# Kernel optimization log

Hardware: AMD Instinct MI355X
Metric: run time of the kernel (lower is better)

Reference implementation:

```python
import jax, jax.numpy as jnp
import numpy as np

DIM, WIDTH, TOTAL, BATCH, NSLOTS = 4096, 4, 16384, 8, 256


def setup_inputs() -> dict:
    key = jax.random.key(0)
    ks = jax.random.split(key, 6)
    x = jax.random.normal(ks[0], (DIM, TOTAL), dtype=jnp.float32)
    weight = jax.random.normal(ks[1], (DIM, WIDTH), dtype=jnp.float32) * 0.1
    conv_states = jax.random.normal(ks[2], (NSLOTS, DIM, WIDTH - 1), dtype=jnp.float32)
    cuts = jnp.sort(jax.random.randint(ks[3], (BATCH - 1,), 1, TOTAL)).astype(jnp.int32)
    query_start_loc = jnp.concatenate([
        jnp.zeros((1,), jnp.int32), cuts, jnp.full((1,), TOTAL, jnp.int32)])
    cache_indices = jax.random.permutation(ks[4], NSLOTS)[:BATCH].astype(jnp.int32)
    initial_state_mode = jax.random.randint(ks[5], (BATCH,), 0, 2).astype(jnp.int32)
    return dict(x=x, weight=weight, conv_states=conv_states,
                query_start_loc=query_start_loc, cache_indices=cache_indices,
                initial_state_mode=initial_state_mode,
                pad_slot_id=-1, residual_connection=1)


def _causal_conv1d_varlen(x, weight, conv_states, qsl, cache_indices, init_mode,
                          pad_slot_id, residual_connection):
    dim, T = x.shape
    width = weight.shape[1]
    state_len = width - 1
    nslots = conv_states.shape[0]
    B = qsl.shape[0] - 1

    t = jnp.arange(T)
    # sequence id and local position of every packed token
    seg = jnp.clip(jnp.searchsorted(qsl, t, side='right') - 1, 0, B - 1)  # [T]
    p = t - qsl[seg]                                                      # [T] local pos
    raw_slot = cache_indices[seg]
    valid_slot = raw_slot != pad_slot_id
    slot = jnp.where(valid_slot, raw_slot, 0)
    use_init = (init_mode[seg] != 0) & valid_slot                         # [T]

    # depthwise causal conv: out[:,t] = sum_k w[:,k] * concat(init_state, x_seq)[:, p+k]
    out = jnp.zeros_like(x)
    for k in range(width):
        d = width - 1 - k  # lookback distance
        if d == 0:
            val = x
        else:
            in_seq = p >= d
            vx = x[:, jnp.clip(t - d, 0, T - 1)]                          # [dim,T]
            st_idx = jnp.clip(state_len - d + p, 0, state_len - 1)        # [T]
            vs = conv_states[slot, :, st_idx].T                           # [dim,T]
            val = jnp.where(in_seq[None, :], vx,
                            jnp.where(use_init[None, :], vs, 0.0))
        out = out + weight[:, k:k + 1] * val

    if residual_connection:
        out = out + x

    # updated cache: last state_len entries of concat(init_state, x_seq) per sequence
    j = jnp.arange(state_len)                                             # [S]
    start, end = qsl[:-1], qsl[1:]
    L = end - start                                                       # [B]
    gx = end[:, None] + j[None, :] - state_len                            # [B,S] global idx
    from_x = gx >= start[:, None]                                         # [B,S]
    sidx = jnp.clip(L[:, None] + j[None, :], 0, state_len - 1)            # [B,S]
    b_valid = cache_indices != pad_slot_id
    b_slot = jnp.where(b_valid, cache_indices, 0)
    b_init = (init_mode != 0) & b_valid
    vx_new = x[:, jnp.clip(gx, 0, T - 1)]                                 # [dim,B,S]
    vs_new = jnp.transpose(conv_states[b_slot[:, None], :, sidx], (2, 0, 1))  # [dim,B,S]
    init_vals = jnp.where(b_init[None, :, None], vs_new, 0.0)
    new_states = jnp.where(from_x[None, :, :], vx_new, init_vals)         # [dim,B,S]
    new_states = jnp.transpose(new_states, (1, 0, 2))                     # [B,dim,S]

    # scatter (pad_slot_id rows go to a throwaway extra slot)
    cs_ext = jnp.concatenate(
        [conv_states, jnp.zeros((1, dim, state_len), conv_states.dtype)], axis=0)
    scatter_idx = jnp.where(b_valid, cache_indices, nslots)
    cs_ext = cs_ext.at[scatter_idx].set(new_states)
    return out, cs_ext[:nslots]


def reference(x, weight, conv_states, query_start_loc, cache_indices,
              initial_state_mode, pad_slot_id, residual_connection):
    return _causal_conv1d_varlen(x, weight, conv_states, query_start_loc,
                                 cache_indices, initial_state_mode,
                                 pad_slot_id, residual_connection)
```

## Files before the change

### kernel.cpp

```cpp
#include <hip/hip_runtime.h>

#define DIM 4096
#define TOTAL 16384
#define STATE_LEN 3
#define BATCH 8
#define NSLOTS 256
#define TVEC (TOTAL / 4)
#define NCONV4 (DIM * TVEC)
#define SROW (DIM * STATE_LEN)
#define S4_PER_SLOT (SROW / 4)
#define NSTATE4 (NSLOTS * S4_PER_SLOT)
#define NBLK 2048
#define NTHREADS (NBLK * 256)

typedef float floatx4 __attribute__((ext_vector_type(4)));

__global__ __launch_bounds__(256) void fused_kernel(
    const float* __restrict__ x, const float* __restrict__ weight,
    const float* __restrict__ cs, const int* __restrict__ qsl,
    const int* __restrict__ cache_indices, const int* __restrict__ init_mode,
    const int* __restrict__ pad_p, const int* __restrict__ res_p,
    float* __restrict__ out, float* __restrict__ out_states)
{
    int q[BATCH + 1];
    #pragma unroll
    for (int k = 0; k <= BATCH; k++) q[k] = qsl[k];
    int ci_[BATCH], im_[BATCH];
    #pragma unroll
    for (int k = 0; k < BATCH; k++) { ci_[k] = cache_indices[k]; im_[k] = init_mode[k]; }
    const int pad = pad_p[0];
    const float wres = res_p[0] ? 1.0f : 0.0f;

    const int tid = blockIdx.x * 256 + threadIdx.x;
    const floatx4* __restrict__ x4 = (const floatx4*)x;
    const floatx4* __restrict__ cs4 = (const floatx4*)cs;

    for (int f = tid; f < NSTATE4; f += NTHREADS) {
        int slot = f / S4_PER_SLOT;
        floatx4 cv = cs4[f];
        bool found = false; int start = 0, end = 0, imv = 0;
        #pragma unroll
        for (int k = 0; k < BATCH; k++) {
            bool m = (ci_[k] == slot) && (ci_[k] != pad);
            start = m ? q[k] : start;
            end   = m ? q[k + 1] : end;
            imv   = m ? im_[k] : imv;
            found = found || m;
        }
        if (!found) {
            __builtin_nontemporal_store(cv, (floatx4*)out_states + f);
        } else {
            int L = end - start;
            bool init = (imv != 0);
            int base = (f - slot * S4_PER_SLOT) * 4;
            float r[4];
            #pragma unroll
            for (int e = 0; e < 4; e++) {
                int idx = base + e;
                int d = idx / 3;
                int j = idx - d * 3;
                int gx = end + j - STATE_LEN;
                float val;
                if (gx >= start) {
                    val = x[(size_t)d * TOTAL + gx];
                } else if (init) {
                    int sidx = L + j;
                    if (sidx > STATE_LEN - 1) sidx = STATE_LEN - 1;
                    val = cs[(size_t)slot * SROW + d * STATE_LEN + sidx];
                } else {
                    val = 0.f;
                }
                r[e] = val;
            }
            floatx4 rv = (floatx4){r[0], r[1], r[2], r[3]};
            __builtin_nontemporal_store(rv, (floatx4*)out_states + f);
        }
    }

    #pragma unroll 2
    for (int v = tid; v < NCONV4; v += NTHREADS) {
        int d  = v >> 12;
        int tv = v & (TVEC - 1);
        int t0 = tv << 2;

        floatx4 cur = x4[v];
        int pv = (tv > 0) ? (v - 1) : v;
        floatx4 prev = x4[pv];
        if (tv == 0) prev = (floatx4){0.f, 0.f, 0.f, 0.f};

        floatx4 w = ((const floatx4*)weight)[d];
        w.w += wres;

        float win[7] = {prev.y, prev.z, prev.w, cur.x, cur.y, cur.z, cur.w};

        int qs_lo = 0, qs_hi = 0;
        #pragma unroll
        for (int k = 1; k < BATCH; k++) {
            qs_lo = (t0     >= q[k]) ? q[k] : qs_lo;
            qs_hi = (t0 + 3 >= q[k]) ? q[k] : qs_hi;
        }

        floatx4 o;
        if ((qs_lo == qs_hi) && (t0 - qs_lo >= 3)) {
            o.x = w.x * win[0] + w.y * win[1] + w.z * win[2] + w.w * win[3];
            o.y = w.x * win[1] + w.y * win[2] + w.z * win[3] + w.w * win[4];
            o.z = w.x * win[2] + w.y * win[3] + w.z * win[4] + w.w * win[5];
            o.w = w.x * win[3] + w.y * win[4] + w.z * win[5] + w.w * win[6];
        } else {
            float res4[4];
            #pragma unroll
            for (int ii = 0; ii < 4; ii++) {
                int t = t0 + ii;
                int qs = 0, civ = ci_[0], imv = im_[0];
                #pragma unroll
                for (int k = 1; k < BATCH; k++) {
                    bool m = (t >= q[k]);
                    qs  = m ? q[k]   : qs;
                    civ = m ? ci_[k] : civ;
                    imv = m ? im_[k] : imv;
                }
                int p = t - qs;
                float xt = win[3 + ii];
                float acc;
                if (p >= 3) {
                    acc = w.x * win[ii] + w.y * win[ii + 1] + w.z * win[ii + 2] + w.w * xt;
                } else {
                    bool valid = (civ != pad);
                    int slot = valid ? civ : 0;
                    bool use_init = valid && (imv != 0);
                    const float* csrow = cs + ((size_t)slot * DIM + d) * STATE_LEN;
                    float xm1 = (p >= 1) ? win[ii + 2] : (use_init ? csrow[2 + p] : 0.f);
                    float xm2 = (p >= 2) ? win[ii + 1] : (use_init ? csrow[1 + p] : 0.f);
                    float xm3 =                          (use_init ? csrow[0 + p] : 0.f);
                    acc = w.x * xm3 + w.y * xm2 + w.z * xm1 + w.w * xt;
                }
                res4[ii] = acc;
            }
            o = (floatx4){res4[0], res4[1], res4[2], res4[3]};
        }
        __builtin_nontemporal_store(o, (floatx4*)out + v);
    }
}

extern "C" void kernel_launch(void* const* d_in, const int* in_sizes, int n_in,
                              void* d_out, int out_size, void* d_ws, size_t ws_size,
                              hipStream_t stream) {
    const float* x      = (const float*)d_in[0];
    const float* weight = (const float*)d_in[1];
    const float* cs     = (const float*)d_in[2];
    const int*   qsl    = (const int*)d_in[3];
    const int*   ci     = (const int*)d_in[4];
    const int*   im     = (const int*)d_in[5];
    const int*   pad    = (const int*)d_in[6];
    const int*   res    = (const int*)d_in[7];

    float* out        = (float*)d_out;
    float* out_states = out + (size_t)DIM * TOTAL;

    fused_kernel<<<NBLK, 256, 0, stream>>>(
        x, weight, cs, qsl, ci, im, pad, res, out, out_states);
}
```

Before: 516.2 us.

## Split conv and state work into dedicated blocks with 16 outputs per thread

Replaces the grid-stride loop with a launch sized to the work: one set of blocks computes 16 consecutive conv outputs per thread, another set handles the state rows. Each thread loads four adjacent float4s plus one halo vector, which cuts redundant halo loads and the per-element loop overhead. The batch metadata is loaded only in the slow boundary path. Per-thread loads are now strided by 64 bytes across lanes, which may hurt coalescing per instruction, and register use goes up.

```diff
diff --git a/kernel.cpp b/kernel.cpp
--- a/kernel.cpp
+++ b/kernel.cpp
@@ -6,12 +6,12 @@
 #define BATCH 8
 #define NSLOTS 256
 #define TVEC (TOTAL / 4)
-#define NCONV4 (DIM * TVEC)
+#define F4PB 1024
+#define CONV_BLKS ((DIM * TVEC) / F4PB)
 #define SROW (DIM * STATE_LEN)
 #define S4_PER_SLOT (SROW / 4)
 #define NSTATE4 (NSLOTS * S4_PER_SLOT)
-#define NBLK 2048
-#define NTHREADS (NBLK * 256)
+#define STATE_BLKS (NSTATE4 / 256)
 
 typedef float floatx4 __attribute__((ext_vector_type(4)));
 
@@ -22,29 +22,102 @@
     const int* __restrict__ pad_p, const int* __restrict__ res_p,
     float* __restrict__ out, float* __restrict__ out_states)
 {
-    int q[BATCH + 1];
-    #pragma unroll
-    for (int k = 0; k <= BATCH; k++) q[k] = qsl[k];
-    int ci_[BATCH], im_[BATCH];
-    #pragma unroll
-    for (int k = 0; k < BATCH; k++) { ci_[k] = cache_indices[k]; im_[k] = init_mode[k]; }
-    const int pad = pad_p[0];
-    const float wres = res_p[0] ? 1.0f : 0.0f;
+    if (blockIdx.x < CONV_BLKS) {
+        const int d   = blockIdx.x >> 2;
+        const int tvb = ((blockIdx.x & 3) << 10) | (threadIdx.x << 2);
+        const int t0  = tvb << 2;
 
-    const int tid = blockIdx.x * 256 + threadIdx.x;
-    const floatx4* __restrict__ x4 = (const floatx4*)x;
-    const floatx4* __restrict__ cs4 = (const floatx4*)cs;
+        const floatx4* __restrict__ xr = (const floatx4*)x + (size_t)d * TVEC;
+        floatx4 c0 = xr[tvb + 0];
+        floatx4 c1 = xr[tvb + 1];
+        floatx4 c2 = xr[tvb + 2];
+        floatx4 c3 = xr[tvb + 3];
+        floatx4 pv = xr[(tvb > 0) ? (tvb - 1) : 0];
+        if (tvb == 0) pv = (floatx4){0.f, 0.f, 0.f, 0.f};
 
-    for (int f = tid; f < NSTATE4; f += NTHREADS) {
-        int slot = f / S4_PER_SLOT;
-        floatx4 cv = cs4[f];
+        int q[BATCH + 1];
+        #pragma unroll
+        for (int k = 0; k <= BATCH; k++) q[k] = qsl[k];
+
+        floatx4 w = ((const floatx4*)weight)[d];
+        w.w += res_p[0] ? 1.0f : 0.0f;
+
+        float win[19] = {pv.y, pv.z, pv.w,
+                         c0.x, c0.y, c0.z, c0.w,
+                         c1.x, c1.y, c1.z, c1.w,
+                         c2.x, c2.y, c2.z, c2.w,
+                         c3.x, c3.y, c3.z, c3.w};
+
+        int qs_lo = 0, qs_hi = 0;
+        #pragma unroll
+        for (int k = 1; k < BATCH; k++) {
+            qs_lo = (t0      >= q[k]) ? q[k] : qs_lo;
+            qs_hi = (t0 + 15 >= q[k]) ? q[k] : qs_hi;
+        }
+
+        float res[16];
+        if ((qs_lo == qs_hi) && (t0 - qs_lo >= 3)) {
+            #pragma unroll
+            for (int j = 0; j < 16; j++)
+                res[j] = w.x * win[j] + w.y * win[j + 1] + w.z * win[j + 2] + w.w * win[j + 3];
+        } else {
+            const int pad = pad_p[0];
+            int ci_[BATCH], im_[BATCH];
+            #pragma unroll
+            for (int k = 0; k < BATCH; k++) { ci_[k] = cache_indices[k]; im_[k] = init_mode[k]; }
+            #pragma unroll
+            for (int j = 0; j < 16; j++) {
+                const int t = t0 + j;
+                int qs = 0, civ = ci_[0], imv = im_[0];
+                #pragma unroll
+                for (int k = 1; k < BATCH; k++) {
+                    bool m = (t >= q[k]);
+                    qs  = m ? q[k]   : qs;
+                    civ = m ? ci_[k] : civ;
+                    imv = m ? im_[k] : imv;
+                }
+                const int p = t - qs;
+                const float xt = win[3 + j];
+                float acc;
+                if (p >= 3) {
+                    acc = w.x * win[j] + w.y * win[j + 1] + w.z * win[j + 2] + w.w * xt;
+                } else {
+                    bool valid = (civ != pad);
+                    int slot = valid ? civ : 0;
+                    bool use_init = valid && (imv != 0);
+                    const float* csrow = cs + ((size_t)slot * DIM + d) * STATE_LEN;
+                    float xm1 = (p >= 1) ? win[j + 2] : (use_init ? csrow[2 + p] : 0.f);
+                    float xm2 = (p >= 2) ? win[j + 1] : (use_init ? csrow[1 + p] : 0.f);
+                    float xm3 =                          (use_init ? csrow[0 + p] : 0.f);
+                    acc = w.x * xm3 + w.y * xm2 + w.z * xm1 + w.w * xt;
+                }
+                res[j] = acc;
+            }
+        }
+
+        floatx4* orow = (floatx4*)out + (size_t)d * TVEC;
+        __builtin_nontemporal_store((floatx4){res[0],  res[1],  res[2],  res[3]},  orow + tvb + 0);
+        __builtin_nontemporal_store((floatx4){res[4],  res[5],  res[6],  res[7]},  orow + tvb + 1);
+        __builtin_nontemporal_store((floatx4){res[8],  res[9],  res[10], res[11]}, orow + tvb + 2);
+        __builtin_nontemporal_store((floatx4){res[12], res[13], res[14], res[15]}, orow + tvb + 3);
+    } else {
+        const int f = (blockIdx.x - CONV_BLKS) * 256 + threadIdx.x;
+        const int slot = f / S4_PER_SLOT;
+        floatx4 cv = ((const floatx4*)cs)[f];
+
+        int q[BATCH + 1];
+        #pragma unroll
+        for (int k = 0; k <= BATCH; k++) q[k] = qsl[k];
+        const int pad = pad_p[0];
+
         bool found = false; int start = 0, end = 0, imv = 0;
         #pragma unroll
         for (int k = 0; k < BATCH; k++) {
-            bool m = (ci_[k] == slot) && (ci_[k] != pad);
-            start = m ? q[k] : start;
+            int cik = cache_indices[k];
+            bool m = (cik == slot) && (cik != pad);
+            start = m ? q[k]     : start;
             end   = m ? q[k + 1] : end;
-            imv   = m ? im_[k] : imv;
+            imv   = m ? init_mode[k] : imv;
             found = found || m;
         }
         if (!found) {
@@ -72,73 +145,9 @@
                 }
                 r[e] = val;
             }
-            floatx4 rv = (floatx4){r[0], r[1], r[2], r[3]};
-            __builtin_nontemporal_store(rv, (floatx4*)out_states + f);
+            __builtin_nontemporal_store((floatx4){r[0], r[1], r[2], r[3]},
+                                        (floatx4*)out_states + f);
         }
-    }
-
-    #pragma unroll 2
-    for (int v = tid; v < NCONV4; v += NTHREADS) {
-        int d  = v >> 12;
-        int tv = v & (TVEC - 1);
-        int t0 = tv << 2;
-
-        floatx4 cur = x4[v];
-        int pv = (tv > 0) ? (v - 1) : v;
-        floatx4 prev = x4[pv];
-        if (tv == 0) prev = (floatx4){0.f, 0.f, 0.f, 0.f};
-
-        floatx4 w = ((const floatx4*)weight)[d];
-        w.w += wres;
-
-        float win[7] = {prev.y, prev.z, prev.w, cur.x, cur.y, cur.z, cur.w};
-
-        int qs_lo = 0, qs_hi = 0;
-        #pragma unroll
-        for (int k = 1; k < BATCH; k++) {
-            qs_lo = (t0     >= q[k]) ? q[k] : qs_lo;
-            qs_hi = (t0 + 3 >= q[k]) ? q[k] : qs_hi;
-        }
-
-        floatx4 o;
-        if ((qs_lo == qs_hi) && (t0 - qs_lo >= 3)) {
-            o.x = w.x * win[0] + w.y * win[1] + w.z * win[2] + w.w * win[3];
-            o.y = w.x * win[1] + w.y * win[2] + w.z * win[3] + w.w * win[4];
-            o.z = w.x * win[2] + w.y * win[3] + w.z * win[4] + w.w * win[5];
-            o.w = w.x * win[3] + w.y * win[4] + w.z * win[5] + w.w * win[6];
-        } else {
-            float res4[4];
-            #pragma unroll
-            for (int ii = 0; ii < 4; ii++) {
-                int t = t0 + ii;
-                int qs = 0, civ = ci_[0], imv = im_[0];
-                #pragma unroll
-                for (int k = 1; k < BATCH; k++) {
-                    bool m = (t >= q[k]);
-                    qs  = m ? q[k]   : qs;
-                    civ = m ? ci_[k] : civ;
-                    imv = m ? im_[k] : imv;
-                }
-                int p = t - qs;
-                float xt = win[3 + ii];
-                float acc;
-                if (p >= 3) {
-                    acc = w.x * win[ii] + w.y * win[ii + 1] + w.z * win[ii + 2] + w.w * xt;
-                } else {
-                    bool valid = (civ != pad);
-                    int slot = valid ? civ : 0;
-                    bool use_init = valid && (imv != 0);
-                    const float* csrow = cs + ((size_t)slot * DIM + d) * STATE_LEN;
-                    float xm1 = (p >= 1) ? win[ii + 2] : (use_init ? csrow[2 + p] : 0.f);
-                    float xm2 = (p >= 2) ? win[ii + 1] : (use_init ? csrow[1 + p] : 0.f);
-                    float xm3 =                          (use_init ? csrow[0 + p] : 0.f);
-                    acc = w.x * xm3 + w.y * xm2 + w.z * xm1 + w.w * xt;
-                }
-                res4[ii] = acc;
-            }
-            o = (floatx4){res4[0], res4[1], res4[2], res4[3]};
-        }
-        __builtin_nontemporal_store(o, (floatx4*)out + v);
     }
 }
 
@@ -157,6 +166,6 @@
     float* out        = (float*)d_out;
     float* out_states = out + (size_t)DIM * TOTAL;
 
-    fused_kernel<<<NBLK, 256, 0, stream>>>(
+    fused_kernel<<<CONV_BLKS + STATE_BLKS, 256, 0, stream>>>(
         x, weight, cs, qsl, ci, im, pad, res, out, out_states);
 }
```

New measurement: 589.5 us. 14.2% more time.
